# Kernel tuning notes

Hardware: AMD Instinct MI355X
Metric: run time of the kernel (lower is better)

The kernel has to match this reference:

```python
import jax, jax.numpy as jnp
import numpy as np

VOCAB = 32000
EMBED = 256
HIDDEN = 512
BATCH = 64
SEQ = 512


def setup_inputs() -> dict:
    key = jax.random.key(0)
    k1, k2, k3, k4, k5, k6 = jax.random.split(key, 6)
    s = 1.0 / np.sqrt(HIDDEN)
    return {
        "source": jax.random.randint(k1, (BATCH, SEQ), 0, VOCAB),
        "embedding": jax.random.normal(k2, (VOCAB, EMBED), dtype=jnp.float32),
        "W_ih": jax.random.uniform(k3, (EMBED, HIDDEN), dtype=jnp.float32, minval=-s, maxval=s),
        "W_hh": jax.random.uniform(k4, (HIDDEN, HIDDEN), dtype=jnp.float32, minval=-s, maxval=s),
        "b_ih": jax.random.uniform(k5, (HIDDEN,), dtype=jnp.float32, minval=-s, maxval=s),
        "b_hh": jax.random.uniform(k6, (HIDDEN,), dtype=jnp.float32, minval=-s, maxval=s),
    }


def reference(source, embedding, W_ih, W_hh, b_ih, b_hh):
    # Embedding lookup: (B, S, E)
    embedded = embedding[source]
    batch_size = source.shape[0]
    h0 = jnp.zeros((batch_size, HIDDEN), dtype=embedding.dtype)

    def step(h, x_t):
        # Elman RNN cell: h' = tanh(x W_ih + b_ih + h W_hh + b_hh)
        h_new = jnp.tanh(x_t @ W_ih + b_ih + h @ W_hh + b_hh)
        return h_new, h_new

    # scan over time axis: xs shape (S, B, E)
    _, hiddens = jax.lax.scan(step, h0, jnp.swapaxes(embedded, 0, 1))
    # hiddens: (S, B, H) -> (B, S, H)
    return jnp.swapaxes(hiddens, 0, 1)
```

## Files before the change

kernel.cpp:

```cpp
#include <hip/hip_runtime.h>
#include <stdint.h>

#define EMBED  256
#define HIDDEN 512
#define BATCH  64
#define SEQ    512

typedef _Float16 f16x8 __attribute__((ext_vector_type(8)));
typedef _Float16 f16x4 __attribute__((ext_vector_type(4)));
typedef float    f32x4 __attribute__((ext_vector_type(4)));


#define WIH_FRAGS (8 * 32 * 64 * 8)
#define WHH_FRAGS (16 * 32 * 64 * 8)

__global__ void prep_pack(const float* __restrict__ W_ih,
                          const float* __restrict__ W_hh,
                          unsigned short* __restrict__ wih_p,
                          unsigned short* __restrict__ whh_p) {
    int tid = blockIdx.x * blockDim.x + threadIdx.x;
    if (tid < WIH_FRAGS) {
        int j = tid & 7, l = (tid >> 3) & 63, nt = (tid >> 9) & 31, s = tid >> 14;
        int k   = s * 32 + ((l >> 4) << 3) + j;
        int col = (nt << 4) + (l & 15);
        wih_p[tid] = __builtin_bit_cast(unsigned short, (_Float16)W_ih[k * HIDDEN + col]);
    } else {
        int t2 = tid - WIH_FRAGS;
        if (t2 < WHH_FRAGS) {
            int j = t2 & 7, l = (t2 >> 3) & 63, mt = (t2 >> 9) & 31, s = t2 >> 14;
            int k   = s * 32 + ((l >> 4) << 3) + j;
            int col = (mt << 4) + (l & 15);
            whh_p[t2] = __builtin_bit_cast(unsigned short, (_Float16)W_hh[k * HIDDEN + col]);
        }
    }
}

__global__ __launch_bounds__(256) void enc_gemm_ih(
    const int* __restrict__ source,
    const float* __restrict__ embedding,
    const unsigned short* __restrict__ wih_p,
    const float* __restrict__ b_ih,
    const float* __restrict__ b_hh,
    float* __restrict__ out)
{
    const int lane = threadIdx.x & 63;
    const int mt   = (blockIdx.x << 2) + (threadIdx.x >> 6);
    const int r0   = mt << 4;
    const int g    = lane >> 4;
    const int c    = lane & 15;

    const int idx = source[r0 + c];
    const float* erow = embedding + (size_t)idx * EMBED;

    f16x8 afrag[8];
#pragma unroll
    for (int s = 0; s < 8; ++s) {
        const float* p = erow + (s << 5) + (g << 3);
        f32x4 f0 = *(const f32x4*)p;
        f32x4 f1 = *(const f32x4*)(p + 4);
        f16x8 a;
        a[0] = (_Float16)f0[0]; a[1] = (_Float16)f0[1];
        a[2] = (_Float16)f0[2]; a[3] = (_Float16)f0[3];
        a[4] = (_Float16)f1[0]; a[5] = (_Float16)f1[1];
        a[6] = (_Float16)f1[2]; a[7] = (_Float16)f1[3];
        afrag[s] = a;
    }

    const f16x8* wp = (const f16x8*)wih_p;
    for (int nt = 0; nt < 32; ++nt) {
        f32x4 acc = {0.f, 0.f, 0.f, 0.f};
#pragma unroll
        for (int s = 0; s < 8; ++s) {
            f16x8 bfr = wp[(((s << 5) + nt) << 6) + lane];
            acc = __builtin_amdgcn_mfma_f32_16x16x32_f16(afrag[s], bfr, acc, 0, 0, 0);
        }
        const int col  = (nt << 4) + c;
        const float bias = b_ih[col] + b_hh[col];
        char* ob = (char*)out + (size_t)(r0 + (g << 2)) * 2048 + 1024 + (col << 1);
#pragma unroll
        for (int r = 0; r < 4; ++r)
            *(_Float16*)(ob + (size_t)r * 2048) = (_Float16)(acc[r] + bias);
    }
}

__global__ __launch_bounds__(512, 2) void enc_rnn(
    const unsigned short* __restrict__ whh_p,
    float* __restrict__ out)
{
    extern __shared__ char lds[];
    char* hbase = lds;
    char* wbase = lds + 32768;

    const int tid  = threadIdx.x;
    const int lane = tid & 63;
    const int w    = tid >> 6;
    const int g    = lane >> 4;
    const int c    = lane & 15;
    const int cx   = c & 7;
    const int mtg0 = w << 2;

    const f16x8* wp = (const f16x8*)whh_p;

    {
        char* wl = wbase + ((w * 12) << 10) + (lane << 4);
#pragma unroll
        for (int fid = 0; fid < 12; ++fid) {
            int s = 9 + (fid >> 2), m = fid & 3;
            f16x8 v = wp[((s * 32 + mtg0 + m) << 6) + lane];
            *(f16x8*)(wl + (fid << 10)) = v;
        }
    }
    for (int i = tid; i < 32768 / 4; i += 512) ((int*)hbase)[i] = 0;

    f16x8 wreg[9][4];
#pragma unroll
    for (int s = 0; s < 9; ++s)
#pragma unroll
        for (int m = 0; m < 4; ++m)
            wreg[s][m] = wp[((s * 32 + mtg0 + m) << 6) + lane];

    __syncthreads();

    const int ch = cx >> 2;
    char* hb2  = hbase + (c << 10) + ((g ^ (cx & 3)) << 4);
    char* hbev = hb2 + (ch << 6);
    char* hbod = hb2 - (ch << 6);
    char* hw[4];
#pragma unroll
    for (int m = 0; m < 4; ++m) {
        int chunk = (w << 3) | ((m ^ (cx >> 1)) << 1) | ((g >> 1) ^ (cx & 1));
        hw[m] = hbase + (c << 10) + (chunk << 4) + ((g & 1) << 3);
    }
    const int b = (blockIdx.x << 4) + c;
    char* gaddr = (char*)out + (size_t)b * SEQ * (HIDDEN * 4) + (w << 7) + (g << 3);
    const char* sp[4];
#pragma unroll
    for (int s = 0; s < 4; ++s)
        sp[s] = (const char*)whh_p + (((12 + s) * 32 + mtg0) << 10) + (lane << 4);
    char* wl = wbase + ((w * 12) << 10) + (lane << 4);

    auto STEP = [&](int RB, int RBN, int TB) {
        f16x8 sA[4], sB[4];
#pragma unroll
        for (int m = 0; m < 4; ++m) sA[m] = *(const f16x8*)(sp[0] + (m << 10));
#pragma unroll
        for (int m = 0; m < 4; ++m) sB[m] = *(const f16x8*)(sp[1] + (m << 10));
        f16x4 pre[4];
#pragma unroll
        for (int m = 0; m < 4; ++m)
            pre[m] = *(const f16x4*)(gaddr + TB + 1024 + (m << 5));

        f32x4 acc[4];
#pragma unroll
        for (int m = 0; m < 4; ++m) acc[m] = (f32x4){0.f, 0.f, 0.f, 0.f};

#pragma unroll
        for (int s = 0; s < 9; ++s) {
            f16x8 h = *(const f16x8*)(((s & 1) ? hbod : hbev) + (s << 6) + RB);
#pragma unroll
            for (int m = 0; m < 4; ++m)
                acc[m] = __builtin_amdgcn_mfma_f32_16x16x32_f16(wreg[s][m], h, acc[m], 0, 0, 0);
        }
#pragma unroll
        for (int s = 9; s < 12; ++s) {
            f16x8 h = *(const f16x8*)(((s & 1) ? hbod : hbev) + (s << 6) + RB);
#pragma unroll
            for (int m = 0; m < 4; ++m) {
                f16x8 wv = *(const f16x8*)(wl + ((((s - 9) << 2) | m) << 10));
                acc[m] = __builtin_amdgcn_mfma_f32_16x16x32_f16(wv, h, acc[m], 0, 0, 0);
            }
        }
        {
            f16x8 h = *(const f16x8*)(hbev + (12 << 6) + RB);
#pragma unroll
            for (int m = 0; m < 4; ++m)
                acc[m] = __builtin_amdgcn_mfma_f32_16x16x32_f16(sA[m], h, acc[m], 0, 0, 0);
        }
#pragma unroll
        for (int m = 0; m < 4; ++m) sA[m] = *(const f16x8*)(sp[2] + (m << 10));
        {
            f16x8 h = *(const f16x8*)(hbod + (13 << 6) + RB);
#pragma unroll
            for (int m = 0; m < 4; ++m)
                acc[m] = __builtin_amdgcn_mfma_f32_16x16x32_f16(sB[m], h, acc[m], 0, 0, 0);
        }
#pragma unroll
        for (int m = 0; m < 4; ++m) sB[m] = *(const f16x8*)(sp[3] + (m << 10));
        {
            f16x8 h = *(const f16x8*)(hbev + (14 << 6) + RB);
#pragma unroll
            for (int m = 0; m < 4; ++m)
                acc[m] = __builtin_amdgcn_mfma_f32_16x16x32_f16(sA[m], h, acc[m], 0, 0, 0);
        }
        {
            f16x8 h = *(const f16x8*)(hbod + (15 << 6) + RB);
#pragma unroll
            for (int m = 0; m < 4; ++m)
                acc[m] = __builtin_amdgcn_mfma_f32_16x16x32_f16(sB[m], h, acc[m], 0, 0, 0);
        }

#pragma unroll
        for (int m = 0; m < 4; ++m) {
            f16x4 hv;
#pragma unroll
            for (int r = 0; r < 4; ++r) {
                float x  = acc[m][r] + (float)pre[m][r];
                float e  = __expf(2.0f * x);
                float th = 1.0f - 2.0f * __builtin_amdgcn_rcpf(e + 1.0f);
                hv[r] = (_Float16)th;
            }
            *(f16x4*)(gaddr + TB + (m << 5)) = hv;
            *(f16x4*)(hw[m] + RBN) = hv;
        }
        __syncthreads();
    };

#pragma unroll 1
    for (int tp = 0; tp < SEQ; tp += 2) {
        STEP(0, 16384, 0);
        STEP(16384, 0, 2048);
        gaddr += 4096;
    }
}

__global__ __launch_bounds__(256) void expand_rows(float* __restrict__ out) {
    const int lane = threadIdx.x & 63;
    const int row  = (blockIdx.x << 2) + (threadIdx.x >> 6);
    char* rp = (char*)out + ((size_t)row << 11);
    f16x8 v = *(const f16x8*)(rp + (lane << 4));
    f32x4 lo, hi;
#pragma unroll
    for (int i = 0; i < 4; ++i) { lo[i] = (float)v[i]; hi[i] = (float)v[i + 4]; }
    *(f32x4*)(rp + (lane << 5))      = lo;
    *(f32x4*)(rp + (lane << 5) + 16) = hi;
}

extern "C" void kernel_launch(void* const* d_in, const int* in_sizes, int n_in,
                              void* d_out, int out_size, void* d_ws, size_t ws_size,
                              hipStream_t stream) {
    const int*   source    = (const int*)d_in[0];
    const float* embedding = (const float*)d_in[1];
    const float* W_ih      = (const float*)d_in[2];
    const float* W_hh      = (const float*)d_in[3];
    const float* b_ih      = (const float*)d_in[4];
    const float* b_hh      = (const float*)d_in[5];
    float* out = (float*)d_out;

    unsigned short* wih_p = (unsigned short*)d_ws;
    unsigned short* whh_p = wih_p + WIH_FRAGS;

    prep_pack<<<(WIH_FRAGS + WHH_FRAGS) / 256, 256, 0, stream>>>(W_ih, W_hh, wih_p, whh_p);
    enc_gemm_ih<<<512, 256, 0, stream>>>(source, embedding, wih_p, b_ih, b_hh, out);
    enc_rnn<<<4, 512, 131072, stream>>>(whh_p, out);
    expand_rows<<<8192, 256, 0, stream>>>(out);
}
```

Measured before the change: 1.299 ms.

## Split recurrent RNN across 8 blocks of 8 batches with more LDS-resident weights

The recurrent kernel now launches 8 blocks, each handling 8 batch rows instead of 16, so more CUs run the sequential scan in parallel. The 16-wide MFMA columns are half idle (lanes with c>=8 duplicate work and skip the stores). LDS now holds 18 weight fragments per wave instead of 12, registers hold 34 instead of 36, and only 3 slices are streamed from global each step. Hidden-state loads are software-pipelined two slices ahead. The cost is wasted MFMA throughput and fewer live registers (launch bounds now 1 block per CU), in exchange for shorter per-step latency spread over more CUs.

```diff
diff --git a/kernel.cpp b/kernel.cpp
--- a/kernel.cpp
+++ b/kernel.cpp
@@ -83,120 +83,104 @@
     }
 }
 
-__global__ __launch_bounds__(512, 2) void enc_rnn(
+__global__ __launch_bounds__(512, 1) void enc_rnn(
     const unsigned short* __restrict__ whh_p,
     float* __restrict__ out)
 {
     extern __shared__ char lds[];
     char* hbase = lds;
-    char* wbase = lds + 32768;
+    char* wbase = lds + 16384;
 
     const int tid  = threadIdx.x;
     const int lane = tid & 63;
     const int w    = tid >> 6;
     const int g    = lane >> 4;
     const int c    = lane & 15;
-    const int cx   = c & 7;
+    const int cc   = lane & 7;
+    const bool cvalid = (c < 8);
     const int mtg0 = w << 2;
 
     const f16x8* wp = (const f16x8*)whh_p;
 
     {
-        char* wl = wbase + ((w * 12) << 10) + (lane << 4);
-#pragma unroll
-        for (int fid = 0; fid < 12; ++fid) {
-            int s = 9 + (fid >> 2), m = fid & 3;
+        char* wl = wbase + ((w * 18) << 10) + (lane << 4);
+#pragma unroll
+        for (int fid = 0; fid < 18; ++fid) {
+            int s = (fid < 2) ? 8 : 9 + ((fid - 2) >> 2);
+            int m = (fid < 2) ? 2 + fid : ((fid - 2) & 3);
             f16x8 v = wp[((s * 32 + mtg0 + m) << 6) + lane];
             *(f16x8*)(wl + (fid << 10)) = v;
         }
     }
-    for (int i = tid; i < 32768 / 4; i += 512) ((int*)hbase)[i] = 0;
-
-    f16x8 wreg[9][4];
-#pragma unroll
-    for (int s = 0; s < 9; ++s)
+    for (int i = tid; i < 16384 / 4; i += 512) ((int*)hbase)[i] = 0;
+
+    f16x8 wreg[34];
+#pragma unroll
+    for (int s = 0; s < 8; ++s)
 #pragma unroll
         for (int m = 0; m < 4; ++m)
-            wreg[s][m] = wp[((s * 32 + mtg0 + m) << 6) + lane];
+            wreg[s * 4 + m] = wp[((s * 32 + mtg0 + m) << 6) + lane];
+#pragma unroll
+    for (int m = 0; m < 2; ++m)
+        wreg[32 + m] = wp[((8 * 32 + mtg0 + m) << 6) + lane];
 
     __syncthreads();
 
-    const int ch = cx >> 2;
-    char* hb2  = hbase + (c << 10) + ((g ^ (cx & 3)) << 4);
-    char* hbev = hb2 + (ch << 6);
-    char* hbod = hb2 - (ch << 6);
+    char* hev = hbase + (cc << 10) + ((cc >> 2) << 6) + ((g ^ (cc & 3)) << 4);
+    char* hod = hbase + (cc << 10) + (((cc >> 2) ^ 1) << 6) + ((g ^ (cc & 3)) << 4);
     char* hw[4];
 #pragma unroll
     for (int m = 0; m < 4; ++m) {
-        int chunk = (w << 3) | ((m ^ (cx >> 1)) << 1) | ((g >> 1) ^ (cx & 1));
-        hw[m] = hbase + (c << 10) + (chunk << 4) + ((g & 1) << 3);
-    }
-    const int b = (blockIdx.x << 4) + c;
-    char* gaddr = (char*)out + (size_t)b * SEQ * (HIDDEN * 4) + (w << 7) + (g << 3);
-    const char* sp[4];
-#pragma unroll
-    for (int s = 0; s < 4; ++s)
-        sp[s] = (const char*)whh_p + (((12 + s) * 32 + mtg0) << 10) + (lane << 4);
-    char* wl = wbase + ((w * 12) << 10) + (lane << 4);
+        int u = (w << 3) + (m << 1) + (g >> 1);
+        hw[m] = hbase + (cc << 10) + ((u ^ cc) << 4) + ((g & 1) << 3);
+    }
+    char* ga = (char*)out + (size_t)((blockIdx.x << 3) + cc) * SEQ * 2048
+             + (w << 7) + (g << 3);
+    const char* sp0 = (const char*)whh_p + ((13 * 32 + mtg0) << 10) + (lane << 4);
+    const char* sp1 = (const char*)whh_p + ((14 * 32 + mtg0) << 10) + (lane << 4);
+    const char* sp2 = (const char*)whh_p + ((15 * 32 + mtg0) << 10) + (lane << 4);
+    char* wl = wbase + ((w * 18) << 10) + (lane << 4);
 
     auto STEP = [&](int RB, int RBN, int TB) {
-        f16x8 sA[4], sB[4];
-#pragma unroll
-        for (int m = 0; m < 4; ++m) sA[m] = *(const f16x8*)(sp[0] + (m << 10));
-#pragma unroll
-        for (int m = 0; m < 4; ++m) sB[m] = *(const f16x8*)(sp[1] + (m << 10));
+        f16x8 sA[4], sB[4], sC[4];
+#pragma unroll
+        for (int m = 0; m < 4; ++m) sA[m] = *(const f16x8*)(sp0 + (m << 10));
+#pragma unroll
+        for (int m = 0; m < 4; ++m) sB[m] = *(const f16x8*)(sp1 + (m << 10));
         f16x4 pre[4];
 #pragma unroll
         for (int m = 0; m < 4; ++m)
-            pre[m] = *(const f16x4*)(gaddr + TB + 1024 + (m << 5));
+            pre[m] = *(const f16x4*)(ga + TB + 1024 + (m << 5));
 
         f32x4 acc[4];
 #pragma unroll
         for (int m = 0; m < 4; ++m) acc[m] = (f32x4){0.f, 0.f, 0.f, 0.f};
 
-#pragma unroll
-        for (int s = 0; s < 9; ++s) {
-            f16x8 h = *(const f16x8*)(((s & 1) ? hbod : hbev) + (s << 6) + RB);
-#pragma unroll
-            for (int m = 0; m < 4; ++m)
-                acc[m] = __builtin_amdgcn_mfma_f32_16x16x32_f16(wreg[s][m], h, acc[m], 0, 0, 0);
-        }
-#pragma unroll
-        for (int s = 9; s < 12; ++s) {
-            f16x8 h = *(const f16x8*)(((s & 1) ? hbod : hbev) + (s << 6) + RB);
+        f16x8 hh[16];
+        hh[0] = *(const f16x8*)(hev + RB);
+        hh[1] = *(const f16x8*)(hod + (0 << 7) + RB);
+#pragma unroll
+        for (int s = 0; s < 16; ++s) {
+            if (s + 2 < 16) {
+                int sn = s + 2;
+                hh[sn] = *(const f16x8*)(((sn & 1) ? hod : hev) + ((sn >> 1) << 7) + RB);
+            }
+            if (s == 9) {
+#pragma unroll
+                for (int m = 0; m < 4; ++m) sC[m] = *(const f16x8*)(sp2 + (m << 10));
+            }
 #pragma unroll
             for (int m = 0; m < 4; ++m) {
-                f16x8 wv = *(const f16x8*)(wl + ((((s - 9) << 2) | m) << 10));
-                acc[m] = __builtin_amdgcn_mfma_f32_16x16x32_f16(wv, h, acc[m], 0, 0, 0);
-            }
-        }
-        {
-            f16x8 h = *(const f16x8*)(hbev + (12 << 6) + RB);
-#pragma unroll
-            for (int m = 0; m < 4; ++m)
-                acc[m] = __builtin_amdgcn_mfma_f32_16x16x32_f16(sA[m], h, acc[m], 0, 0, 0);
-        }
-#pragma unroll
-        for (int m = 0; m < 4; ++m) sA[m] = *(const f16x8*)(sp[2] + (m << 10));
-        {
-            f16x8 h = *(const f16x8*)(hbod + (13 << 6) + RB);
-#pragma unroll
-            for (int m = 0; m < 4; ++m)
-                acc[m] = __builtin_amdgcn_mfma_f32_16x16x32_f16(sB[m], h, acc[m], 0, 0, 0);
-        }
-#pragma unroll
-        for (int m = 0; m < 4; ++m) sB[m] = *(const f16x8*)(sp[3] + (m << 10));
-        {
-            f16x8 h = *(const f16x8*)(hbev + (14 << 6) + RB);
-#pragma unroll
-            for (int m = 0; m < 4; ++m)
-                acc[m] = __builtin_amdgcn_mfma_f32_16x16x32_f16(sA[m], h, acc[m], 0, 0, 0);
-        }
-        {
-            f16x8 h = *(const f16x8*)(hbod + (15 << 6) + RB);
-#pragma unroll
-            for (int m = 0; m < 4; ++m)
-                acc[m] = __builtin_amdgcn_mfma_f32_16x16x32_f16(sB[m], h, acc[m], 0, 0, 0);
+                f16x8 wv;
+                if (s < 8)            wv = wreg[s * 4 + m];
+                else if (s == 8 && m < 2) wv = wreg[32 + m];
+                else if (s == 8)      wv = *(const f16x8*)(wl + ((m - 2) << 10));
+                else if (s < 13)      wv = *(const f16x8*)(wl + ((2 + ((s - 9) << 2) + m) << 10));
+                else if (s == 13)     wv = sA[m];
+                else if (s == 14)     wv = sB[m];
+                else                  wv = sC[m];
+                acc[m] = __builtin_amdgcn_mfma_f32_16x16x32_f16(wv, hh[s], acc[m], 0, 0, 0);
+            }
         }
 
 #pragma unroll
@@ -209,17 +193,19 @@
                 float th = 1.0f - 2.0f * __builtin_amdgcn_rcpf(e + 1.0f);
                 hv[r] = (_Float16)th;
             }
-            *(f16x4*)(gaddr + TB + (m << 5)) = hv;
-            *(f16x4*)(hw[m] + RBN) = hv;
+            if (cvalid) {
+                *(f16x4*)(ga + TB + (m << 5)) = hv;
+                *(f16x4*)(hw[m] + RBN) = hv;
+            }
         }
         __syncthreads();
     };
 
 #pragma unroll 1
     for (int tp = 0; tp < SEQ; tp += 2) {
-        STEP(0, 16384, 0);
-        STEP(16384, 0, 2048);
-        gaddr += 4096;
+        STEP(0, 8192, 0);
+        STEP(8192, 0, 2048);
+        ga += 4096;
     }
 }
 
@@ -251,6 +237,6 @@
 
     prep_pack<<<(WIH_FRAGS + WHH_FRAGS) / 256, 256, 0, stream>>>(W_ih, W_hh, wih_p, whh_p);
     enc_gemm_ih<<<512, 256, 0, stream>>>(source, embedding, wih_p, b_ih, b_hh, out);
-    enc_rnn<<<4, 512, 131072, stream>>>(whh_p, out);
+    enc_rnn<<<8, 512, 163840, stream>>>(whh_p, out);
     expand_rows<<<8192, 256, 0, stream>>>(out);
 }
```

Result: faster. 1.082 ms (-16.7%).
